# Optimization experiments

Hardware: AMD Instinct MI355X
Metric: run time of the kernel (lower is better)

Reference implementation:

```python
import jax, jax.numpy as jnp
import numpy as np

B = 256        # batch of LLR frames
N = 576        # code length (from wman_N0576_R34_z24)
MR = 144       # check rows = N * (1 - 3/4)
Z = 24         # lifting factor
IT = 3         # decoding iterations
ROW_DEG = 15   # check-node degree (WiMAX rate-3/4)


def setup_inputs() -> dict:
    key = jax.random.key(0)
    r = jax.random.normal(key, (B, N), dtype=jnp.float32)
    # Deterministic sparse Tanner graph: 15 ones per check row (>=2 required for top-2)
    rng = np.random.RandomState(0)
    Hnp = np.zeros((MR, N), dtype=np.int32)
    cols = np.argsort(rng.rand(MR, N), axis=1)[:, :ROW_DEG]
    Hnp[np.arange(MR)[:, None], cols] = 1
    H = jnp.asarray(Hnp)
    alpha = jnp.ones((MR // Z, N // Z, IT), dtype=jnp.float32) * 0.7
    beta = jnp.ones((MR // Z, N // Z, IT), dtype=jnp.float32) * 0.05
    return {"r": r, "alpha": alpha, "beta": beta, "H": H}


def _decode(r, alpha, beta, Hf):
    # r: (B, N) channel LLRs; Hf: (MR, N) float 0/1 parity-check mask
    mask = Hf == 1.0
    node = jnp.arange(N)[None, None, :]           # (1, 1, N)
    M = Hf[None, :, :] * r[:, None, :]            # initial v->c messages (B, MR, N)
    E = jnp.zeros_like(M)
    n_it = alpha.shape[-1]
    for it in range(n_it):
        a = jnp.repeat(jnp.repeat(alpha[:, :, it], Z, axis=0), Z, axis=1)  # (MR, N)
        bt = jnp.repeat(jnp.repeat(beta[:, :, it], Z, axis=0), Z, axis=1)  # (MR, N)
        # check -> variable: masked min-2 magnitude + extrinsic sign product
        abs_M = jnp.abs(M)
        masked = jnp.where(mask, abs_M, jnp.inf)
        neg_vals, idx = jax.lax.top_k(-masked, 2)  # two smallest per check row
        min_vals = -neg_vals                        # (B, MR, 2)
        # exclude self: use 2nd min at the argmin position, 1st min elsewhere
        E_abs = jnp.where(node == idx[..., 0:1], min_vals[..., 1:2], min_vals[..., 0:1])
        signs = jnp.where(mask, jnp.sign(M), 1.0)
        row_sign_prod = jnp.prod(signs, axis=2, keepdims=True)
        E_sign = row_sign_prod * signs              # extrinsic sign
        E = a * E_sign * jax.nn.relu(E_abs - bt) * Hf
        # variable -> check: sum-minus-self
        sum_E = jnp.sum(E, axis=1, keepdims=True)   # (B, 1, N)
        M = (r[:, None, :] + sum_E - E) * Hf
    return r + jnp.sum(E, axis=1)                   # posterior LLRs (B, N)


def reference(r, alpha, beta, H):
    return _decode(r, alpha, beta, H.astype(jnp.float32))
```

## Files before the change

### kernel.cpp

```cpp
#include <hip/hip_runtime.h>

#define BATCH   256
#define NCOL    576
#define MROW    144
#define ZLIFT   24
#define NIT     3
#define ROW_DEG 15
#define NEDGE   (MROW * ROW_DEG)
#define NSCIT   ((MROW/ZLIFT) * (NCOL/ZLIFT) * NIT)
#define TPB     512

__global__ __launch_bounds__(256) void build_cols_kernel(
    const int* __restrict__ H, int* __restrict__ pk)
{
    const int wave = (blockIdx.x * blockDim.x + threadIdx.x) >> 6;
    const int lane = threadIdx.x & 63;
    if (wave >= MROW) return;
    const int4* row4 = (const int4*)(H + (size_t)wave * NCOL);
    const int srow = (wave / ZLIFT) * (NCOL / ZLIFT);
    const unsigned long long below = (1ull << lane) - 1ull;
    int base = 0;
    #pragma unroll
    for (int r0 = 0; r0 < 3; ++r0) {
        const int vidx = r0 * 64 + lane;
        int4 h = make_int4(0, 0, 0, 0);
        if (vidx < NCOL / 4) h = row4[vidx];
        const int b0 = h.x != 0, b1 = h.y != 0, b2 = h.z != 0, b3 = h.w != 0;
        const unsigned long long m0 = __ballot(b0);
        const unsigned long long m1 = __ballot(b1);
        const unsigned long long m2 = __ballot(b2);
        const unsigned long long m3 = __ballot(b3);
        const int cnt_below = __popcll(m0 & below) + __popcll(m1 & below)
                            + __popcll(m2 & below) + __popcll(m3 & below);
        const int bits[4] = {b0, b1, b2, b3};
        const int n0 = vidx * 4;
        int pref = 0;
        #pragma unroll
        for (int c = 0; c < 4; ++c) {
            if (bits[c]) {
                const int idx = base + cnt_below + pref;
                const int n = n0 + c;
                if (idx < ROW_DEG)
                    pk[wave * ROW_DEG + idx] = n | ((srow + n / ZLIFT) << 16);
                ++pref;
            }
        }
        base += __popcll(m0) + __popcll(m1) + __popcll(m2) + __popcll(m3);
    }
}

__global__ __launch_bounds__(TPB) void ldpc_decode_kernel(
    const float* __restrict__ r,
    const float* __restrict__ alpha,
    const float* __restrict__ beta,
    const int*   __restrict__ pk,
    float*       __restrict__ out)
{
    __shared__ float r_s[NCOL];
    __shared__ float colsum[NCOL];
    __shared__ float E_s[NEDGE];
    __shared__ float a_s[NSCIT];
    __shared__ float b_s[NSCIT];
    __shared__ int   cdeg[NCOL];
    __shared__ int   cstart[NCOL];

    const int b   = blockIdx.x;
    const int tid = threadIdx.x;

    for (int n = tid; n < NCOL; n += TPB) {
        r_s[n]  = r[(size_t)b * NCOL + n];
        cdeg[n] = 0;
    }
    if (tid < NSCIT) { a_s[tid] = alpha[tid]; b_s[tid] = beta[tid]; }
    __syncthreads();

    const bool is_row = (tid < MROW);
    int   pk_r[ROW_DEG];
    float r_r[ROW_DEG];
    float E_r[ROW_DEG];
    int   slot_r[ROW_DEG];
    if (is_row) {
        #pragma unroll
        for (int k = 0; k < ROW_DEG; ++k) {
            const int p = pk[tid * ROW_DEG + k];
            pk_r[k] = p;
            const int n = p & 0xFFFF;
            r_r[k]  = r_s[n];
            E_r[k]  = 0.0f;
            slot_r[k] = atomicAdd(&cdeg[n], 1);
        }
    }
    __syncthreads();

    if (tid < 64) {
        int local[9];
        int run = 0;
        #pragma unroll
        for (int j = 0; j < 9; ++j) { local[j] = cdeg[tid * 9 + j]; run += local[j]; }
        int scan = run;
        #pragma unroll
        for (int off = 1; off < 64; off <<= 1) {
            int up = __shfl_up(scan, off);
            if (tid >= off) scan += up;
        }
        int acc = scan - run;
        #pragma unroll
        for (int j = 0; j < 9; ++j) { cstart[tid * 9 + j] = acc; acc += local[j]; }
    }
    __syncthreads();

    if (is_row) {
        #pragma unroll
        for (int k = 0; k < ROW_DEG; ++k)
            slot_r[k] += cstart[pk_r[k] & 0xFFFF];
    }

    for (int it = 0; it < NIT; ++it) {
        if (is_row) {
            float vals[ROW_DEG];
            float min1 = INFINITY, min2 = INFINITY;
            int   kmin = -1;
            float sprod = 1.0f;
            #pragma unroll
            for (int k = 0; k < ROW_DEG; ++k) {
                float v;
                if (it == 0) {
                    v = r_r[k];
                } else {
                    const int n = pk_r[k] & 0xFFFF;
                    v = r_r[k] + colsum[n] - E_r[k];
                }
                vals[k] = v;
                const float av = fabsf(v);
                const float s = (v > 0.0f) ? 1.0f : ((v < 0.0f) ? -1.0f : 0.0f);
                sprod *= s;
                if (av < min1)      { min2 = min1; min1 = av; kmin = k; }
                else if (av < min2) { min2 = av; }
            }
            #pragma unroll
            for (int k = 0; k < ROW_DEG; ++k) {
                const int sidx = pk_r[k] >> 16;
                const float v = vals[k];
                const float s = (v > 0.0f) ? 1.0f : ((v < 0.0f) ? -1.0f : 0.0f);
                const float a  = a_s[sidx * NIT + it];
                const float bt = b_s[sidx * NIT + it];
                const float eabs = (k == kmin) ? min2 : min1;
                float mag = eabs - bt;
                if (mag < 0.0f) mag = 0.0f;
                const float E = a * (sprod * s) * mag;
                E_r[k] = E;
                E_s[slot_r[k]] = E;
            }
        }
        __syncthreads();

        if (it < NIT - 1) {
            for (int n = tid; n < NCOL; n += TPB) {
                const int s0  = cstart[n];
                const int deg = cdeg[n];
                float sum = 0.0f;
                for (int i = 0; i < deg; ++i) sum += E_s[s0 + i];
                colsum[n] = sum;
            }
            __syncthreads();
        } else {
            for (int n = tid; n < NCOL; n += TPB) {
                const int s0  = cstart[n];
                const int deg = cdeg[n];
                float sum = 0.0f;
                for (int i = 0; i < deg; ++i) sum += E_s[s0 + i];
                out[(size_t)b * NCOL + n] = r_s[n] + sum;
            }
        }
    }
}

extern "C" void kernel_launch(void* const* d_in, const int* in_sizes, int n_in,
                              void* d_out, int out_size, void* d_ws, size_t ws_size,
                              hipStream_t stream) {
    const float* r     = (const float*)d_in[0];
    const float* alpha = (const float*)d_in[1];
    const float* beta  = (const float*)d_in[2];
    const int*   H     = (const int*)d_in[3];
    float* out = (float*)d_out;
    int*   pk  = (int*)d_ws;

    build_cols_kernel<<<(MROW * 64 + 255) / 256, 256, 0, stream>>>(H, pk);
    ldpc_decode_kernel<<<BATCH, TPB, 0, stream>>>(r, alpha, beta, pk, out);
}
```

Baseline: 71.45 us.

## Replace CSR column scan with fixed-capacity padded per-column edge slots

Check-to-variable messages are now stored in a fixed-stride per-column slot array of capacity 18 with stride 19, which is zero-filled up front. This removes the shared-memory prefix scan, the `cstart` table and two block barriers. Column sums become fully unrolled reads of all 18 slots instead of a variable-degree loop. Packed row column lists are padded to stride 16 so they can be loaded as int4 vectors. The trade-offs are more LDS use, an extra zero-fill pass, wasted reads of empty slots, and silent overflow if any column degree exceeds 18.

```diff
diff --git a/kernel.cpp b/kernel.cpp
--- a/kernel.cpp
+++ b/kernel.cpp
@@ -6,9 +6,11 @@
 #define ZLIFT   24
 #define NIT     3
 #define ROW_DEG 15
-#define NEDGE   (MROW * ROW_DEG)
+#define PKSTR   16
 #define NSCIT   ((MROW/ZLIFT) * (NCOL/ZLIFT) * NIT)
 #define TPB     512
+#define CCAP    18
+#define CSTR    19
 
 __global__ __launch_bounds__(256) void build_cols_kernel(
     const int* __restrict__ H, int* __restrict__ pk)
@@ -41,7 +43,7 @@
                 const int idx = base + cnt_below + pref;
                 const int n = n0 + c;
                 if (idx < ROW_DEG)
-                    pk[wave * ROW_DEG + idx] = n | ((srow + n / ZLIFT) << 16);
+                    pk[wave * PKSTR + idx] = n | ((srow + n / ZLIFT) << 16);
                 ++pref;
             }
         }
@@ -58,11 +60,10 @@
 {
     __shared__ float r_s[NCOL];
     __shared__ float colsum[NCOL];
-    __shared__ float E_s[NEDGE];
+    __shared__ float E_s[NCOL * CSTR];
     __shared__ float a_s[NSCIT];
     __shared__ float b_s[NSCIT];
     __shared__ int   cdeg[NCOL];
-    __shared__ int   cstart[NCOL];
 
     const int b   = blockIdx.x;
     const int tid = threadIdx.x;
@@ -71,6 +72,7 @@
         r_s[n]  = r[(size_t)b * NCOL + n];
         cdeg[n] = 0;
     }
+    for (int i = tid; i < NCOL * CSTR; i += TPB) E_s[i] = 0.0f;
     if (tid < NSCIT) { a_s[tid] = alpha[tid]; b_s[tid] = beta[tid]; }
     __syncthreads();
 
@@ -80,39 +82,20 @@
     float E_r[ROW_DEG];
     int   slot_r[ROW_DEG];
     if (is_row) {
+        const int4* prow = (const int4*)(pk + tid * PKSTR);
+        int4 q[4];
+        #pragma unroll
+        for (int j = 0; j < 4; ++j) q[j] = prow[j];
+        const int* qi = (const int*)q;
         #pragma unroll
         for (int k = 0; k < ROW_DEG; ++k) {
-            const int p = pk[tid * ROW_DEG + k];
+            const int p = qi[k];
             pk_r[k] = p;
             const int n = p & 0xFFFF;
             r_r[k]  = r_s[n];
             E_r[k]  = 0.0f;
-            slot_r[k] = atomicAdd(&cdeg[n], 1);
+            slot_r[k] = n * CSTR + atomicAdd(&cdeg[n], 1);
         }
-    }
-    __syncthreads();
-
-    if (tid < 64) {
-        int local[9];
-        int run = 0;
-        #pragma unroll
-        for (int j = 0; j < 9; ++j) { local[j] = cdeg[tid * 9 + j]; run += local[j]; }
-        int scan = run;
-        #pragma unroll
-        for (int off = 1; off < 64; off <<= 1) {
-            int up = __shfl_up(scan, off);
-            if (tid >= off) scan += up;
-        }
-        int acc = scan - run;
-        #pragma unroll
-        for (int j = 0; j < 9; ++j) { cstart[tid * 9 + j] = acc; acc += local[j]; }
-    }
-    __syncthreads();
-
-    if (is_row) {
-        #pragma unroll
-        for (int k = 0; k < ROW_DEG; ++k)
-            slot_r[k] += cstart[pk_r[k] & 0xFFFF];
     }
 
     for (int it = 0; it < NIT; ++it) {
@@ -156,19 +139,19 @@
 
         if (it < NIT - 1) {
             for (int n = tid; n < NCOL; n += TPB) {
-                const int s0  = cstart[n];
-                const int deg = cdeg[n];
+                const float* base = &E_s[n * CSTR];
                 float sum = 0.0f;
-                for (int i = 0; i < deg; ++i) sum += E_s[s0 + i];
+                #pragma unroll
+                for (int i = 0; i < CCAP; ++i) sum += base[i];
                 colsum[n] = sum;
             }
             __syncthreads();
         } else {
             for (int n = tid; n < NCOL; n += TPB) {
-                const int s0  = cstart[n];
-                const int deg = cdeg[n];
+                const float* base = &E_s[n * CSTR];
                 float sum = 0.0f;
-                for (int i = 0; i < deg; ++i) sum += E_s[s0 + i];
+                #pragma unroll
+                for (int i = 0; i < CCAP; ++i) sum += base[i];
                 out[(size_t)b * NCOL + n] = r_s[n] + sum;
             }
         }
```

New measurement: 69.74 us. -2.4%, faster.
